# Kernel optimization log

Measured on AMD Instinct MI355X. Metric: run time of the kernel, lower is better.

Reference implementation:

```python
import jax, jax.numpy as jnp
import numpy as np

B, L, D, S = 8, 512, 64, 8


def setup_inputs() -> dict:
    key = jax.random.key(0)
    ks = jax.random.split(key, 8)
    return {
        "lstm1": jax.random.normal(ks[0], (B, L, D), dtype=jnp.float32),
        "lstm2": jax.random.normal(ks[1], (B, L, D), dtype=jnp.float32),
        "W": jax.random.normal(ks[2], (S, D, D), dtype=jnp.float32) * 0.1,
        "V": jax.random.normal(ks[3], (S, 2 * D), dtype=jnp.float32) * 0.1,
        "b": jax.random.normal(ks[4], (S,), dtype=jnp.float32) * 0.1,
        "W_g": jax.random.normal(ks[5], (S, 2 * D), dtype=jnp.float32) * 0.1,
        "b_g": jax.random.normal(ks[6], (S,), dtype=jnp.float32) * 0.1,
        "u": jax.random.normal(ks[7], (1, S), dtype=jnp.float32) * 0.1,
    }


def reference(lstm1, lstm2, W, V, b, W_g, b_g, u):
    # lstm1/lstm2: (B, L, D). Pairwise slot (i, j) pairs lstm1[:, i] with lstm2[:, j].
    d = lstm1.shape[-1]
    # Bilinear tensor-network score: x1_i W_s x2_j -> (B, L, L, S)
    result_w = jnp.einsum('bid,sde,bje->bijs', lstm1, W, lstm2)
    # concat(x1_i, x2_j) @ V^T decomposed to avoid materializing (B,L,L,2D)
    v1 = jnp.einsum('bid,sd->bis', lstm1, V[:, :d])[:, :, None, :]   # (B,L,1,S)
    v2 = jnp.einsum('bjd,sd->bjs', lstm2, V[:, d:])[:, None, :, :]   # (B,1,L,S)
    result_v = v1 + v2                                               # (B,L,L,S)
    g1 = jnp.einsum('bid,sd->bis', lstm1, W_g[:, :d])[:, :, None, :]
    g2 = jnp.einsum('bjd,sd->bjs', lstm2, W_g[:, d:])[:, None, :, :]
    gate = jax.nn.sigmoid(g1 + g2 + b_g)                             # (B,L,L,S)
    result_final = gate * result_w + (1.0 - gate) * jax.nn.sigmoid(result_v) + b
    # Reduce slices with u (shape (1,S)) -> (B,L,L), then add singleton channel dim.
    out = jnp.einsum('bijs,ks->bijk', result_final, u)[..., 0]
    return out[:, None, :, :]  # (B, 1, L, L)
```

## Files before the change

### kernel.cpp

```cpp
#include <hip/hip_runtime.h>
#include <math.h>

typedef float f32x4 __attribute__((ext_vector_type(4)));
typedef short bf16x8 __attribute__((ext_vector_type(8)));

namespace {
constexpr int kB = 8, kL = 512, kD = 64, kS = 8;
constexpr size_t SCL_OFF = 0;
constexpr size_t WT_OFF  = 524288;
constexpr size_t X1B_OFF = 589824;
constexpr size_t X2B_OFF = 1114112;
constexpr size_t T_OFF   = 1638400;
}

__device__ __forceinline__ unsigned short f2bf(float f) {
    unsigned u = __float_as_uint(f);
    u += 0x7FFFu + ((u >> 16) & 1u);
    return (unsigned short)(u >> 16);
}
__device__ __forceinline__ unsigned pk2(float lo, float hi) {
    return (unsigned)f2bf(lo) | ((unsigned)f2bf(hi) << 16);
}

__global__ __launch_bounds__(256) void grn_prep(
    const float* __restrict__ lstm1, const float* __restrict__ lstm2,
    const float* __restrict__ W, const float* __restrict__ V,
    const float* __restrict__ Wg, const float* __restrict__ bg,
    unsigned char* __restrict__ ws)
{
    float* scl = (float*)(ws + SCL_OFF);
    unsigned short* wt = (unsigned short*)(ws + WT_OFF);
    const int tid = threadIdx.x;
    if (blockIdx.x < 8) {
        const int s = blockIdx.x;
        __shared__ float wsm[64][68];
        const float* pw = W + s * 4096;
        const int row = tid >> 2, c0 = (tid & 3) * 16;
        #pragma unroll
        for (int q = 0; q < 4; q++)
            *(float4*)&wsm[row][c0 + q * 4] = *(const float4*)(pw + row * 64 + c0 + q * 4);
        __syncthreads();
        const int e = tid >> 2, d0 = (tid & 3) * 16;
        unsigned wd[8];
        #pragma unroll
        for (int q = 0; q < 8; q++)
            wd[q] = pk2(wsm[d0 + 2 * q][e], wsm[d0 + 2 * q + 1][e]);
        unsigned short* dst = wt + s * 4096 + e * 64 + d0;
        uint4 a = {wd[0], wd[1], wd[2], wd[3]};
        uint4 c = {wd[4], wd[5], wd[6], wd[7]};
        *(uint4*)(dst) = a;
        *(uint4*)(dst + 8) = c;
    } else if (blockIdx.x < 72) {
        const int rb = blockIdx.x - 8;
        const int b = rb >> 3, r0 = (rb & 7) * 64;
        const int kind = tid & 3, row = r0 + (tid >> 2);
        const float* x = (kind < 2 ? lstm1 : lstm2) + ((size_t)b * kL + row) * kD;
        float xr[64];
        #pragma unroll
        for (int q = 0; q < 16; q++)
            *(float4*)&xr[q * 4] = *(const float4*)(x + q * 4);
        const float* vb = ((kind & 1) ? Wg : V) + ((kind & 2) ? kD : 0);
        #pragma unroll
        for (int s = 0; s < kS; s++) {
            const float* vec = vb + s * 2 * kD;
            float a = 0.f;
            #pragma unroll
            for (int q = 0; q < 16; q++) {
                const float4 vv = *(const float4*)(vec + q * 4);
                a = fmaf(vv.x, xr[q * 4 + 0], a);
                a = fmaf(vv.y, xr[q * 4 + 1], a);
                a = fmaf(vv.z, xr[q * 4 + 2], a);
                a = fmaf(vv.w, xr[q * 4 + 3], a);
            }
            const float badd = (kind == 1) ? bg[s] : 0.f;
            scl[(((size_t)kind * 8 + b) * 8 + s) * 512 + row] = __expf(-(a + badd));
        }
    } else {
        const int t = blockIdx.x - 72;
        const float* src = (t < 16) ? lstm1 : lstm2;
        unsigned short* dst = (unsigned short*)(ws + ((t < 16) ? X1B_OFF : X2B_OFF));
        const int tt = (t & 15) * 256 + tid;
        #pragma unroll
        for (int k = 0; k < 8; k++) {
            const int c = tt + k * 4096;
            const float* p = src + (size_t)c * 8;
            const float4 a = *(const float4*)p;
            const float4 b2 = *(const float4*)(p + 4);
            uint4 o = {pk2(a.x, a.y), pk2(a.z, a.w), pk2(b2.x, b2.y), pk2(b2.z, b2.w)};
            *(uint4*)(dst + (size_t)c * 8) = o;
        }
    }
}

__global__ __launch_bounds__(256) void grn_t2(unsigned char* __restrict__ ws)
{
    const unsigned short* wt  = (const unsigned short*)(ws + WT_OFF);
    const unsigned short* x1b = (const unsigned short*)(ws + X1B_OFF);
    unsigned short* T = (unsigned short*)(ws + T_OFF);
    const int g = blockIdx.x * 4 + (threadIdx.x >> 6);
    const int b = g >> 8, rem = g & 255, s = rem >> 5, i16 = rem & 31;
    const int lane = threadIdx.x & 63, fr = lane & 15, fh = lane >> 4;
    const unsigned short* ap = x1b + (((size_t)b * kL + i16 * 16 + fr) * kD + fh * 8);
    bf16x8 A0 = *(const bf16x8*)ap;
    bf16x8 A1 = *(const bf16x8*)(ap + 32);
    const unsigned short* bp = wt + (s * 4096 + fr * 64 + fh * 8);
    unsigned short* tp = T + (((size_t)(b * 8 + s)) * kL + i16 * 16) * kD;
    #pragma unroll
    for (int ne = 0; ne < 4; ne++) {
        const bf16x8 B0 = *(const bf16x8*)(bp + ne * 16 * 64);
        const bf16x8 B1 = *(const bf16x8*)(bp + ne * 16 * 64 + 32);
        f32x4 z = {0.f, 0.f, 0.f, 0.f};
        f32x4 t = __builtin_amdgcn_mfma_f32_16x16x32_bf16(A0, B0, z, 0, 0, 0);
        t = __builtin_amdgcn_mfma_f32_16x16x32_bf16(A1, B1, t, 0, 0, 0);
        #pragma unroll
        for (int r = 0; r < 4; r++)
            tp[(fh * 4 + r) * kD + ne * 16 + fr] = f2bf(t[r]);
    }
}

__global__ __launch_bounds__(256) void grn_m3(
    const float* __restrict__ bS, const float* __restrict__ u,
    const unsigned char* __restrict__ ws, float* __restrict__ out)
{
    const float* scl = (const float*)(ws + SCL_OFF);
    const unsigned short* x2b = (const unsigned short*)(ws + X2B_OFF);
    const unsigned short* T = (const unsigned short*)(ws + T_OFF);
    const int g = blockIdx.x * 4 + (threadIdx.x >> 6);
    const int b = g >> 10, rem = g & 1023, it = rem >> 5, jt = rem & 31;
    const int lane = threadIdx.x & 63, fr = lane & 15, fh = lane >> 4;
    const int i0 = it * 16, j0 = jt * 16;
    const unsigned short* bp = x2b + (((size_t)b * kL + j0 + fr) * kD + fh * 8);
    const bf16x8 Bf0 = *(const bf16x8*)bp;
    const bf16x8 Bf1 = *(const bf16x8*)(bp + 32);
    float bias_c = 0.f;
    #pragma unroll
    for (int s = 0; s < kS; s++) bias_c = fmaf(u[s], bS[s], bias_c);
    f32x4 oacc = {bias_c, bias_c, bias_c, bias_c};
    #pragma unroll
    for (int s = 0; s < kS; s++) {
        const unsigned short* ap = T + (((size_t)(b * 8 + s)) * kL + i0 + fr) * kD + fh * 8;
        const bf16x8 A0 = *(const bf16x8*)ap;
        const bf16x8 A1 = *(const bf16x8*)(ap + 32);
        f32x4 z = {0.f, 0.f, 0.f, 0.f};
        f32x4 acc = __builtin_amdgcn_mfma_f32_16x16x32_bf16(A0, Bf0, z, 0, 0, 0);
        acc = __builtin_amdgcn_mfma_f32_16x16x32_bf16(A1, Bf1, acc, 0, 0, 0);
        const float4 E1vq = *(const float4*)(scl + (((size_t)0 * 8 + b) * 8 + s) * 512 + i0 + fh * 4);
        const float4 E1gq = *(const float4*)(scl + (((size_t)1 * 8 + b) * 8 + s) * 512 + i0 + fh * 4);
        const float E2v = scl[(((size_t)2 * 8 + b) * 8 + s) * 512 + j0 + fr];
        const float E2g = scl[(((size_t)3 * 8 + b) * 8 + s) * 512 + j0 + fr];
        const float us = u[s];
        const float E1va[4] = {E1vq.x, E1vq.y, E1vq.z, E1vq.w};
        const float E1ga[4] = {E1gq.x, E1gq.y, E1gq.z, E1gq.w};
        #pragma unroll
        for (int r = 0; r < 4; r++) {
            const float dg = fmaf(E1ga[r], E2g, 1.f);
            const float dv = fmaf(E1va[r], E2v, 1.f);
            const float rp = __builtin_amdgcn_rcpf(dg * dv);
            const float gate = dv * rp;
            const float sv   = dg * rp;
            const float res = fmaf(gate, acc[r] - sv, sv);
            oacc[r] = fmaf(us, res, oacc[r]);
        }
    }
    float* op = out + (((size_t)b * kL + i0 + fh * 4) * kL + j0 + fr);
    #pragma unroll
    for (int r = 0; r < 4; r++)
        op[(size_t)r * kL] = oacc[r];
}

extern "C" void kernel_launch(void* const* d_in, const int* in_sizes, int n_in,
                              void* d_out, int out_size, void* d_ws, size_t ws_size,
                              hipStream_t stream) {
    const float* lstm1 = (const float*)d_in[0];
    const float* lstm2 = (const float*)d_in[1];
    const float* W     = (const float*)d_in[2];
    const float* V     = (const float*)d_in[3];
    const float* bS    = (const float*)d_in[4];
    const float* Wg    = (const float*)d_in[5];
    const float* bg    = (const float*)d_in[6];
    const float* u     = (const float*)d_in[7];
    unsigned char* ws = (unsigned char*)d_ws;
    grn_prep<<<104, 256, 0, stream>>>(lstm1, lstm2, W, V, Wg, bg, ws);
    grn_t2<<<512, 256, 0, stream>>>(ws);
    grn_m3<<<2048, 256, 0, stream>>>(bS, u, ws, (float*)d_out);
}
```

Measured before the change: 113.2 us.

## Fuse prep and T computation into one kernel and widen final tile

Merges the prep and T-projection kernels into one launch. Each block converts W to bf16 in shared memory and converts lstm1 inline, then stages T through LDS for coalesced stores. The bf16 copies of lstm1/lstm2 in the workspace are gone, and the final kernel converts lstm2 on load. The final kernel now handles two 16-column j tiles per wave, reusing the T fragments and E1 scales, with half as many blocks. This removes one launch and a workspace round trip, at the cost of redundant W conversion per block and more registers.

Measured after the change: 105.2 us. 7.1% less time.

```diff
diff --git a/kernel.cpp b/kernel.cpp
--- a/kernel.cpp
+++ b/kernel.cpp
@@ -7,10 +7,7 @@
 namespace {
 constexpr int kB = 8, kL = 512, kD = 64, kS = 8;
 constexpr size_t SCL_OFF = 0;
-constexpr size_t WT_OFF  = 524288;
-constexpr size_t X1B_OFF = 589824;
-constexpr size_t X2B_OFF = 1114112;
-constexpr size_t T_OFF   = 1638400;
+constexpr size_t T_OFF   = 524288;
 }
 
 __device__ __forceinline__ unsigned short f2bf(float f) {
@@ -21,37 +18,28 @@
 __device__ __forceinline__ unsigned pk2(float lo, float hi) {
     return (unsigned)f2bf(lo) | ((unsigned)f2bf(hi) << 16);
 }
+__device__ __forceinline__ bf16x8 ldcvt8(const float* __restrict__ p) {
+    const float4 a = *(const float4*)p;
+    const float4 b = *(const float4*)(p + 4);
+    union { bf16x8 v; uint4 q; } cv;
+    cv.q.x = pk2(a.x, a.y); cv.q.y = pk2(a.z, a.w);
+    cv.q.z = pk2(b.x, b.y); cv.q.w = pk2(b.z, b.w);
+    return cv.v;
+}
 
-__global__ __launch_bounds__(256) void grn_prep(
+__global__ __launch_bounds__(256) void grn_a(
     const float* __restrict__ lstm1, const float* __restrict__ lstm2,
     const float* __restrict__ W, const float* __restrict__ V,
     const float* __restrict__ Wg, const float* __restrict__ bg,
     unsigned char* __restrict__ ws)
 {
+    __shared__ float wsm[64][68];
+    __shared__ __align__(16) unsigned short tls[4][16][72];
     float* scl = (float*)(ws + SCL_OFF);
-    unsigned short* wt = (unsigned short*)(ws + WT_OFF);
+    unsigned short* T = (unsigned short*)(ws + T_OFF);
     const int tid = threadIdx.x;
-    if (blockIdx.x < 8) {
-        const int s = blockIdx.x;
-        __shared__ float wsm[64][68];
-        const float* pw = W + s * 4096;
-        const int row = tid >> 2, c0 = (tid & 3) * 16;
-        #pragma unroll
-        for (int q = 0; q < 4; q++)
-            *(float4*)&wsm[row][c0 + q * 4] = *(const float4*)(pw + row * 64 + c0 + q * 4);
-        __syncthreads();
-        const int e = tid >> 2, d0 = (tid & 3) * 16;
-        unsigned wd[8];
-        #pragma unroll
-        for (int q = 0; q < 8; q++)
-            wd[q] = pk2(wsm[d0 + 2 * q][e], wsm[d0 + 2 * q + 1][e]);
-        unsigned short* dst = wt + s * 4096 + e * 64 + d0;
-        uint4 a = {wd[0], wd[1], wd[2], wd[3]};
-        uint4 c = {wd[4], wd[5], wd[6], wd[7]};
-        *(uint4*)(dst) = a;
-        *(uint4*)(dst + 8) = c;
-    } else if (blockIdx.x < 72) {
-        const int rb = blockIdx.x - 8;
+    if (blockIdx.x < 64) {
+        const int rb = blockIdx.x;
         const int b = rb >> 3, r0 = (rb & 7) * 64;
         const int kind = tid & 3, row = r0 + (tid >> 2);
         const float* x = (kind < 2 ? lstm1 : lstm2) + ((size_t)b * kL + row) * kD;
@@ -75,97 +63,113 @@
             const float badd = (kind == 1) ? bg[s] : 0.f;
             scl[(((size_t)kind * 8 + b) * 8 + s) * 512 + row] = __expf(-(a + badd));
         }
-    } else {
-        const int t = blockIdx.x - 72;
-        const float* src = (t < 16) ? lstm1 : lstm2;
-        unsigned short* dst = (unsigned short*)(ws + ((t < 16) ? X1B_OFF : X2B_OFF));
-        const int tt = (t & 15) * 256 + tid;
+        return;
+    }
+    const int t = blockIdx.x - 64;
+    const int b = t >> 6, rem = t & 63, s = rem >> 3, i64 = rem & 7;
+    {
+        const float* pw = W + s * 4096;
+        const int row = tid >> 2, c0 = (tid & 3) * 16;
         #pragma unroll
-        for (int k = 0; k < 8; k++) {
-            const int c = tt + k * 4096;
-            const float* p = src + (size_t)c * 8;
-            const float4 a = *(const float4*)p;
-            const float4 b2 = *(const float4*)(p + 4);
-            uint4 o = {pk2(a.x, a.y), pk2(a.z, a.w), pk2(b2.x, b2.y), pk2(b2.z, b2.w)};
-            *(uint4*)(dst + (size_t)c * 8) = o;
-        }
+        for (int q = 0; q < 4; q++)
+            *(float4*)&wsm[row][c0 + q * 4] = *(const float4*)(pw + row * 64 + c0 + q * 4);
     }
+    __syncthreads();
+    const int lane = tid & 63, w = tid >> 6;
+    const int fr = lane & 15, fh = lane >> 4;
+    const int i0 = i64 * 64 + w * 16;
+    const float* ap = lstm1 + (((size_t)b * kL + i0 + fr) * kD + fh * 8);
+    const bf16x8 A0 = ldcvt8(ap);
+    const bf16x8 A1 = ldcvt8(ap + 32);
+    unsigned short (*__restrict__ tw)[72] = tls[w];
+    #pragma unroll
+    for (int ne = 0; ne < 4; ne++) {
+        union { bf16x8 v; uint4 q; } B0, B1;
+        const int e = ne * 16 + fr;
+        B0.q.x = pk2(wsm[fh * 8 + 0][e], wsm[fh * 8 + 1][e]);
+        B0.q.y = pk2(wsm[fh * 8 + 2][e], wsm[fh * 8 + 3][e]);
+        B0.q.z = pk2(wsm[fh * 8 + 4][e], wsm[fh * 8 + 5][e]);
+        B0.q.w = pk2(wsm[fh * 8 + 6][e], wsm[fh * 8 + 7][e]);
+        B1.q.x = pk2(wsm[32 + fh * 8 + 0][e], wsm[32 + fh * 8 + 1][e]);
+        B1.q.y = pk2(wsm[32 + fh * 8 + 2][e], wsm[32 + fh * 8 + 3][e]);
+        B1.q.z = pk2(wsm[32 + fh * 8 + 4][e], wsm[32 + fh * 8 + 5][e]);
+        B1.q.w = pk2(wsm[32 + fh * 8 + 6][e], wsm[32 + fh * 8 + 7][e]);
+        f32x4 z = {0.f, 0.f, 0.f, 0.f};
+        f32x4 d = __builtin_amdgcn_mfma_f32_16x16x32_bf16(A0, B0.v, z, 0, 0, 0);
+        d = __builtin_amdgcn_mfma_f32_16x16x32_bf16(A1, B1.v, d, 0, 0, 0);
+        #pragma unroll
+        for (int r = 0; r < 4; r++)
+            tw[fh * 4 + r][ne * 16 + fr] = f2bf(d[r]);
+    }
+    const int rr = lane >> 2, cc = (lane & 3) * 16;
+    const uint4 q0 = *(const uint4*)&tw[rr][cc];
+    const uint4 q1 = *(const uint4*)&tw[rr][cc + 8];
+    unsigned short* tp = T + (((size_t)(b * 8 + s)) * kL + i0 + rr) * kD + cc;
+    *(uint4*)tp = q0;
+    *(uint4*)(tp + 8) = q1;
 }
 
-__global__ __launch_bounds__(256) void grn_t2(unsigned char* __restrict__ ws)
-{
-    const unsigned short* wt  = (const unsigned short*)(ws + WT_OFF);
-    const unsigned short* x1b = (const unsigned short*)(ws + X1B_OFF);
-    unsigned short* T = (unsigned short*)(ws + T_OFF);
-    const int g = blockIdx.x * 4 + (threadIdx.x >> 6);
-    const int b = g >> 8, rem = g & 255, s = rem >> 5, i16 = rem & 31;
-    const int lane = threadIdx.x & 63, fr = lane & 15, fh = lane >> 4;
-    const unsigned short* ap = x1b + (((size_t)b * kL + i16 * 16 + fr) * kD + fh * 8);
-    bf16x8 A0 = *(const bf16x8*)ap;
-    bf16x8 A1 = *(const bf16x8*)(ap + 32);
-    const unsigned short* bp = wt + (s * 4096 + fr * 64 + fh * 8);
-    unsigned short* tp = T + (((size_t)(b * 8 + s)) * kL + i16 * 16) * kD;
-    #pragma unroll
-    for (int ne = 0; ne < 4; ne++) {
-        const bf16x8 B0 = *(const bf16x8*)(bp + ne * 16 * 64);
-        const bf16x8 B1 = *(const bf16x8*)(bp + ne * 16 * 64 + 32);
-        f32x4 z = {0.f, 0.f, 0.f, 0.f};
-        f32x4 t = __builtin_amdgcn_mfma_f32_16x16x32_bf16(A0, B0, z, 0, 0, 0);
-        t = __builtin_amdgcn_mfma_f32_16x16x32_bf16(A1, B1, t, 0, 0, 0);
-        #pragma unroll
-        for (int r = 0; r < 4; r++)
-            tp[(fh * 4 + r) * kD + ne * 16 + fr] = f2bf(t[r]);
-    }
-}
-
-__global__ __launch_bounds__(256) void grn_m3(
-    const float* __restrict__ bS, const float* __restrict__ u,
-    const unsigned char* __restrict__ ws, float* __restrict__ out)
+__global__ __launch_bounds__(256) void grn_b(
+    const float* __restrict__ lstm2, const float* __restrict__ bS,
+    const float* __restrict__ u, const unsigned char* __restrict__ ws,
+    float* __restrict__ out)
 {
     const float* scl = (const float*)(ws + SCL_OFF);
-    const unsigned short* x2b = (const unsigned short*)(ws + X2B_OFF);
     const unsigned short* T = (const unsigned short*)(ws + T_OFF);
     const int g = blockIdx.x * 4 + (threadIdx.x >> 6);
-    const int b = g >> 10, rem = g & 1023, it = rem >> 5, jt = rem & 31;
+    const int b = g >> 9, rem = g & 511, it = rem >> 4, j32 = rem & 15;
     const int lane = threadIdx.x & 63, fr = lane & 15, fh = lane >> 4;
-    const int i0 = it * 16, j0 = jt * 16;
-    const unsigned short* bp = x2b + (((size_t)b * kL + j0 + fr) * kD + fh * 8);
-    const bf16x8 Bf0 = *(const bf16x8*)bp;
-    const bf16x8 Bf1 = *(const bf16x8*)(bp + 32);
+    const int i0 = it * 16, j0 = j32 * 32;
+    bf16x8 Bf[2][2];
+    #pragma unroll
+    for (int jj = 0; jj < 2; jj++) {
+        const float* bp = lstm2 + (((size_t)b * kL + j0 + jj * 16 + fr) * kD + fh * 8);
+        Bf[jj][0] = ldcvt8(bp);
+        Bf[jj][1] = ldcvt8(bp + 32);
+    }
     float bias_c = 0.f;
     #pragma unroll
     for (int s = 0; s < kS; s++) bias_c = fmaf(u[s], bS[s], bias_c);
-    f32x4 oacc = {bias_c, bias_c, bias_c, bias_c};
+    f32x4 oacc[2];
+    oacc[0] = f32x4{bias_c, bias_c, bias_c, bias_c};
+    oacc[1] = oacc[0];
     #pragma unroll
     for (int s = 0; s < kS; s++) {
         const unsigned short* ap = T + (((size_t)(b * 8 + s)) * kL + i0 + fr) * kD + fh * 8;
         const bf16x8 A0 = *(const bf16x8*)ap;
         const bf16x8 A1 = *(const bf16x8*)(ap + 32);
-        f32x4 z = {0.f, 0.f, 0.f, 0.f};
-        f32x4 acc = __builtin_amdgcn_mfma_f32_16x16x32_bf16(A0, Bf0, z, 0, 0, 0);
-        acc = __builtin_amdgcn_mfma_f32_16x16x32_bf16(A1, Bf1, acc, 0, 0, 0);
         const float4 E1vq = *(const float4*)(scl + (((size_t)0 * 8 + b) * 8 + s) * 512 + i0 + fh * 4);
         const float4 E1gq = *(const float4*)(scl + (((size_t)1 * 8 + b) * 8 + s) * 512 + i0 + fh * 4);
-        const float E2v = scl[(((size_t)2 * 8 + b) * 8 + s) * 512 + j0 + fr];
-        const float E2g = scl[(((size_t)3 * 8 + b) * 8 + s) * 512 + j0 + fr];
         const float us = u[s];
         const float E1va[4] = {E1vq.x, E1vq.y, E1vq.z, E1vq.w};
         const float E1ga[4] = {E1gq.x, E1gq.y, E1gq.z, E1gq.w};
         #pragma unroll
-        for (int r = 0; r < 4; r++) {
-            const float dg = fmaf(E1ga[r], E2g, 1.f);
-            const float dv = fmaf(E1va[r], E2v, 1.f);
-            const float rp = __builtin_amdgcn_rcpf(dg * dv);
-            const float gate = dv * rp;
-            const float sv   = dg * rp;
-            const float res = fmaf(gate, acc[r] - sv, sv);
-            oacc[r] = fmaf(us, res, oacc[r]);
+        for (int jj = 0; jj < 2; jj++) {
+            f32x4 z = {0.f, 0.f, 0.f, 0.f};
+            f32x4 acc = __builtin_amdgcn_mfma_f32_16x16x32_bf16(A0, Bf[jj][0], z, 0, 0, 0);
+            acc = __builtin_amdgcn_mfma_f32_16x16x32_bf16(A1, Bf[jj][1], acc, 0, 0, 0);
+            const int j = j0 + jj * 16 + fr;
+            const float E2v = scl[(((size_t)2 * 8 + b) * 8 + s) * 512 + j];
+            const float E2g = scl[(((size_t)3 * 8 + b) * 8 + s) * 512 + j];
+            #pragma unroll
+            for (int r = 0; r < 4; r++) {
+                const float dg = fmaf(E1ga[r], E2g, 1.f);
+                const float dv = fmaf(E1va[r], E2v, 1.f);
+                const float rp = __builtin_amdgcn_rcpf(dg * dv);
+                const float gate = dv * rp;
+                const float sv   = dg * rp;
+                const float res = fmaf(gate, acc[r] - sv, sv);
+                oacc[jj][r] = fmaf(us, res, oacc[jj][r]);
+            }
         }
     }
-    float* op = out + (((size_t)b * kL + i0 + fh * 4) * kL + j0 + fr);
     #pragma unroll
-    for (int r = 0; r < 4; r++)
-        op[(size_t)r * kL] = oacc[r];
+    for (int jj = 0; jj < 2; jj++) {
+        float* op = out + (((size_t)b * kL + i0 + fh * 4) * kL + j0 + jj * 16 + fr);
+        #pragma unroll
+        for (int r = 0; r < 4; r++)
+            op[(size_t)r * kL] = oacc[jj][r];
+    }
 }
 
 extern "C" void kernel_launch(void* const* d_in, const int* in_sizes, int n_in,
@@ -180,7 +184,6 @@
     const float* bg    = (const float*)d_in[6];
     const float* u     = (const float*)d_in[7];
     unsigned char* ws = (unsigned char*)d_ws;
-    grn_prep<<<104, 256, 0, stream>>>(lstm1, lstm2, W, V, Wg, bg, ws);
-    grn_t2<<<512, 256, 0, stream>>>(ws);
-    grn_m3<<<2048, 256, 0, stream>>>(bS, u, ws, (float*)d_out);
+    grn_a<<<576, 256, 0, stream>>>(lstm1, lstm2, W, V, Wg, bg, ws);
+    grn_b<<<1024, 256, 0, stream>>>(lstm2, bS, u, ws, (float*)d_out);
 }
```
